# Optimization experiments

Hardware: AMD Instinct MI355X
Metric: run time of the kernel (lower is better)

The kernel has to match this reference:

```python
import jax, jax.numpy as jnp
import numpy as np
from jax.scipy.special import logsumexp

EPS = 0.05        # entropic regularization (blur^p)
N_ITERS = 20      # Sinkhorn iterations
N, M, D = 8192, 8192, 64


def setup_inputs() -> dict:
    key = jax.random.key(0)
    k1, k2, k3, k4 = jax.random.split(key, 4)
    return {
        "a": jax.random.uniform(k1, (N,), dtype=jnp.float32),
        "x": jax.random.normal(k2, (N, D), dtype=jnp.float32),
        "b": jax.random.uniform(k3, (M,), dtype=jnp.float32),
        "y": jax.random.normal(k4, (M, D), dtype=jnp.float32),
    }


def reference(a, x, b, y):
    eps = EPS
    # _normalize_weights: probability simplex
    a = a / jnp.sum(a)
    b = b / jnp.sum(b)
    loga = jnp.log(a)
    logb = jnp.log(b)
    # squared-Euclidean cost C_ij = ||x_i - y_j||^2, built via one GEMM (online kernel's math)
    x2 = jnp.sum(x * x, axis=1)            # [N]
    y2 = jnp.sum(y * y, axis=1)            # [M]
    C = x2[:, None] + y2[None, :] - 2.0 * (x @ y.T)   # [N, M]

    # log-domain Sinkhorn: f_i = -eps * LSE_j( log b_j + (g_j - C_ij)/eps )
    def softmin_rows(g_, C_, logw):   # reduce over columns j -> [N]
        return -eps * logsumexp(logw[None, :] + (g_[None, :] - C_) / eps, axis=1)

    def softmin_cols(f_, C_, logw):   # reduce over rows i -> [M]
        return -eps * logsumexp(logw[:, None] + (f_[:, None] - C_) / eps, axis=0)

    def body(i, fg):
        f_, g_ = fg
        f_ = softmin_rows(g_, C, logb)
        g_ = softmin_cols(f_, C, loga)
        return (f_, g_)

    f0 = jnp.zeros_like(a)
    g0 = jnp.zeros_like(b)
    f, g = jax.lax.fori_loop(0, N_ITERS, body, (f0, g0))

    # GeomLoss-style: one final symmetric update from detached potentials (Danskin)
    f_d = jax.lax.stop_gradient(f)
    g_d = jax.lax.stop_gradient(g)
    f_fin = softmin_rows(g_d, C, logb)
    g_fin = softmin_cols(f_d, C, loga)
    # OT_eps(a, b) = <a, f> + <b, g>
    return jnp.sum(a * f_fin) + jnp.sum(b * g_fin)
```

## Files before the change

### kernel.cpp

```cpp
#include <hip/hip_runtime.h>
#include <hip/hip_bf16.h>

#define EPS       0.05f
#define N_ITERS   20
#define NR        8192
#define DIM       64
#define LOG2E     1.4426950408889634f
#define LN2       0.6931471805599453f
#define S2        (2.0f * LOG2E / EPS)
#define EPSLN2    (EPS * LN2)
#define NEGINF    (-1e30f)
#define NSPLIT    16

typedef __attribute__((ext_vector_type(8))) short short8;
typedef __attribute__((ext_vector_type(4))) float float4v;

#define GLD_LDS16(src, dst)                                              \
    __builtin_amdgcn_global_load_lds(                                    \
        (const __attribute__((address_space(1))) void*)(src),            \
        (__attribute__((address_space(3))) void*)(dst), 16, 0, 0)

__device__ __forceinline__ float wave_reduce_sum(float v) {
    #pragma unroll
    for (int m = 1; m < 64; m <<= 1) v += __shfl_xor(v, m, 64);
    return v;
}

__device__ __forceinline__ float merge16_l(const float2* __restrict__ P, int i) {
    float2 p[NSPLIT];
    float M = NEGINF;
    #pragma unroll
    for (int k = 0; k < NSPLIT; k++) {
        p[k] = P[k * NR + i];
        M = fmaxf(M, p[k].x);
    }
    float S = 0.f;
    #pragma unroll
    for (int k = 0; k < NSPLIT; k++)
        S += p[k].y * __builtin_amdgcn_exp2f(p[k].x - M);
    return M + __builtin_amdgcn_logf(S);
}

__global__ void sums_kernel(const float* __restrict__ a, const float* __restrict__ b,
                            float* __restrict__ sums) {
    __shared__ float red[32];
    int tid = threadIdx.x;
    float pa = 0.f, pb = 0.f;
    for (int i = tid; i < NR; i += blockDim.x) { pa += a[i]; pb += b[i]; }
    pa = wave_reduce_sum(pa);
    pb = wave_reduce_sum(pb);
    int wid = tid >> 6, ln = tid & 63;
    if (ln == 0) { red[wid] = pa; red[wid + 16] = pb; }
    __syncthreads();
    if (tid == 0) {
        float sa = 0.f, sb = 0.f;
        int nw = blockDim.x >> 6;
        for (int w = 0; w < nw; w++) { sa += red[w]; sb += red[w + 16]; }
        sums[0] = logf(sa); sums[1] = logf(sb); sums[2] = sa; sums[3] = sb;
    }
}

__global__ void prep_kernel(const float* __restrict__ x, const float* __restrict__ y,
                            const float* __restrict__ a, const float* __restrict__ b,
                            const float* __restrict__ sums,
                            short8* __restrict__ xs, short8* __restrict__ ys,
                            float* __restrict__ x2, float* __restrict__ y2,
                            float* __restrict__ la2, float* __restrict__ lb2,
                            float2* __restrict__ Pb) {
    int gid = blockIdx.x * 256 + threadIdx.x;
    bool isx = gid < NR * 8;
    int cid = isx ? gid : gid - NR * 8;
    int row = cid >> 3;
    int c   = cid & 7;
    const float4* src = (const float4*)(isx ? x : y);
    float4 v0 = src[row * 16 + c * 2];
    float4 v1 = src[row * 16 + c * 2 + 1];

    const float sc = isx ? S2 : 1.0f;
    short8 st;
    st[0] = __bfloat16_as_short(__float2bfloat16(v0.x * sc));
    st[1] = __bfloat16_as_short(__float2bfloat16(v0.y * sc));
    st[2] = __bfloat16_as_short(__float2bfloat16(v0.z * sc));
    st[3] = __bfloat16_as_short(__float2bfloat16(v0.w * sc));
    st[4] = __bfloat16_as_short(__float2bfloat16(v1.x * sc));
    st[5] = __bfloat16_as_short(__float2bfloat16(v1.y * sc));
    st[6] = __bfloat16_as_short(__float2bfloat16(v1.z * sc));
    st[7] = __bfloat16_as_short(__float2bfloat16(v1.w * sc));

    int T = row >> 4, ln = row & 15, f = c >> 2, q = c & 3;
    (isx ? xs : ys)[T * 128 + f * 64 + q * 16 + ln] = st;

    float sq = v0.x*v0.x + v0.y*v0.y + v0.z*v0.z + v0.w*v0.w
             + v1.x*v1.x + v1.y*v1.y + v1.z*v1.z + v1.w*v1.w;
    #pragma unroll
    for (int m = 1; m < 8; m <<= 1) sq += __shfl_xor(sq, m, 64);

    if (c == 0) {
        if (isx) {
            x2[row] = sq;
            la2[row] = (logf(a[row]) - sums[0]) * LOG2E;
        } else {
            y2[row] = sq;
            lb2[row] = (logf(b[row]) - sums[1]) * LOG2E;
            Pb[row] = make_float2(sq * (LOG2E / EPS), 1.0f);
            #pragma unroll
            for (int k = 1; k < NSPLIT; k++)
                Pb[k * NR + row] = make_float2(NEGINF, 0.0f);
        }
    }
}

#define LSE4(acc, mm, ss)                                                \
    {                                                                    \
        float z0 = (acc)[0], z1 = (acc)[1];                              \
        float z2 = (acc)[2], z3 = (acc)[3];                              \
        float mn = fmaxf(fmaxf(fmaxf(z0, z1), fmaxf(z2, z3)), (mm));     \
        float e  = __builtin_amdgcn_exp2f((mm) - mn);                    \
        float p  = (__builtin_amdgcn_exp2f(z0 - mn)                      \
                  + __builtin_amdgcn_exp2f(z1 - mn))                     \
                 + (__builtin_amdgcn_exp2f(z2 - mn)                      \
                  + __builtin_amdgcn_exp2f(z3 - mn));                    \
        (ss) = fmaf((ss), e, p);                                         \
        (mm) = mn;                                                       \
    }

__global__ __launch_bounds__(1024, 4) void pass_kernel(
        const short8* __restrict__ matXs,
        const short8* __restrict__ matYs,
        const float2* __restrict__ Pin,
        const float* __restrict__ lw2col,
        float2* __restrict__ Pout) {
    __shared__ __attribute__((aligned(16))) char xlds[65536];
    __shared__ __attribute__((aligned(16))) char ybuf[4][16384];
    __shared__ __attribute__((aligned(16))) float cbl[512];
    __shared__ float2 comb[512][5];

    const int tid = threadIdx.x;
    const int bi  = blockIdx.x;
    const int q   = bi & 15;
    const int rg  = bi >> 4;
    const int rb  = rg * 512;
    const int cb0 = q * 512;

    const int w    = tid >> 6;
    const int lane = tid & 63;
    const int quad = lane >> 4;
    const int ln   = lane & 15;
    const int cst  = w & 3;
    const int rq   = w >> 2;

    const char* xsrc = (const char*)matXs + (size_t)rb * 128;
    #pragma unroll
    for (int r = 0; r < 4; r++)
        GLD_LDS16(xsrc + r * 16384 + tid * 16, &xlds[r * 16384 + w * 1024]);
    const char* ysrc = (const char*)matYs + (size_t)cb0 * 128;
    #pragma unroll
    for (int c = 0; c < 4; c++)
        GLD_LDS16(ysrc + c * 16384 + tid * 16, &ybuf[c][w * 1024]);
    __builtin_amdgcn_sched_barrier(0);

    if (tid < 512) {
        int j = cb0 + tid;
        cbl[tid] = lw2col[j] - merge16_l(Pin, j);
    }
    __builtin_amdgcn_sched_barrier(0);
    __builtin_amdgcn_s_waitcnt(0x0073);
    __builtin_amdgcn_s_barrier();
    __builtin_amdgcn_sched_barrier(0);

    short8 xf0[8], xf1[8];
    {
        const char* xw = &xlds[(rq * 8) * 2048];
        #pragma unroll
        for (int t = 0; t < 8; t++) {
            xf0[t] = *(const short8*)(xw + t * 2048 + lane * 16);
            xf1[t] = *(const short8*)(xw + t * 2048 + 1024 + lane * 16);
        }
    }

    float lm[8], ls[8];
    #pragma unroll
    for (int t = 0; t < 8; t++) { lm[t] = NEGINF; ls[t] = 0.f; }

    #pragma unroll
    for (int c = 0; c < 4; c++) {
        const char* base = &ybuf[c][0];
        #pragma unroll
        for (int uu = 0; uu < 2; uu++) {
            const int u = cst * 2 + uu;
            short8 ya0 = *(const short8*)(base + u * 2048 + lane * 16);
            short8 ya1 = *(const short8*)(base + u * 2048 + 1024 + lane * 16);
            float4v cin = *(const float4v*)(cbl + (c * 8 + u) * 16 + quad * 4);

            #pragma unroll
            for (int tt = 0; tt < 8; tt++) {
                float4v acc = __builtin_amdgcn_mfma_f32_16x16x32_bf16(ya0, xf0[tt], cin, 0, 0, 0);
                acc = __builtin_amdgcn_mfma_f32_16x16x32_bf16(ya1, xf1[tt], acc, 0, 0, 0);
                LSE4(acc, lm[tt], ls[tt]);
            }
        }
        if (c < 3) {
            __builtin_amdgcn_sched_barrier(0);
            if (c == 0)      __builtin_amdgcn_s_waitcnt(0x0072);
            else if (c == 1) __builtin_amdgcn_s_waitcnt(0x0071);
            else             __builtin_amdgcn_s_waitcnt(0x0070);
            __builtin_amdgcn_s_barrier();
            __builtin_amdgcn_sched_barrier(0);
        }
    }

    #pragma unroll
    for (int mask = 16; mask < 64; mask <<= 1) {
        #pragma unroll
        for (int t = 0; t < 8; t++) {
            float mo = __shfl_xor(lm[t], mask, 64);
            float so = __shfl_xor(ls[t], mask, 64);
            float M  = fmaxf(lm[t], mo);
            ls[t] = ls[t] * __builtin_amdgcn_exp2f(lm[t] - M)
                  + so    * __builtin_amdgcn_exp2f(mo    - M);
            lm[t] = M;
        }
    }

    __syncthreads();
    if (lane < 16) {
        #pragma unroll
        for (int t = 0; t < 8; t++)
            comb[rq * 128 + t * 16 + ln][cst] = make_float2(lm[t], ls[t]);
    }
    __syncthreads();

    if (tid < 512) {
        float2 cc0 = comb[tid][0];
        float M = cc0.x, S = cc0.y;
        #pragma unroll
        for (int cc = 1; cc < 4; cc++) {
            float2 p = comb[tid][cc];
            float Mn = fmaxf(M, p.x);
            S = S * __builtin_amdgcn_exp2f(M - Mn)
              + p.y * __builtin_amdgcn_exp2f(p.x - Mn);
            M = Mn;
        }
        Pout[q * NR + rb + tid] = make_float2(M, S);
    }
}

__global__ void reduce1_kernel(const float* __restrict__ a, const float* __restrict__ b,
                               const float* __restrict__ x2, const float* __restrict__ y2,
                               const float2* __restrict__ Pff, const float2* __restrict__ Pgf,
                               float2* __restrict__ red2) {
    __shared__ float red[4];
    int tid = threadIdx.x;
    int r   = blockIdx.x * 128 + (tid & 127);
    bool gs = tid >= 128;
    float L  = merge16_l(gs ? Pgf : Pff, r);
    float sq = gs ? y2[r] : x2[r];
    float wv = gs ? b[r]  : a[r];
    float v  = wv * (sq - EPSLN2 * L);
    v = wave_reduce_sum(v);
    if ((tid & 63) == 0) red[tid >> 6] = v;
    __syncthreads();
    if (tid == 0) red2[blockIdx.x] = make_float2(red[0] + red[1], red[2] + red[3]);
}

__global__ void reduce2_kernel(const float* __restrict__ sums,
                               const float2* __restrict__ red2,
                               float* __restrict__ out) {
    int tid = threadIdx.x;
    float2 v = red2[tid];
    float da = wave_reduce_sum(v.x);
    float db = wave_reduce_sum(v.y);
    if (tid == 0) out[0] = da / sums[2] + db / sums[3];
}

extern "C" void kernel_launch(void* const* d_in, const int* in_sizes, int n_in,
                              void* d_out, int out_size, void* d_ws, size_t ws_size,
                              hipStream_t stream) {
    const float* a = (const float*)d_in[0];
    const float* x = (const float*)d_in[1];
    const float* b = (const float*)d_in[2];
    const float* y = (const float*)d_in[3];

    char* ws = (char*)d_ws;
    short8* xs = (short8*)ws;
    short8* ys = (short8*)(ws + (1 << 20));
    float* fp  = (float*)(ws + (2 << 20));
    float* x2  = fp;
    float* y2  = fp + NR;
    float* la2 = fp + 2 * NR;
    float* lb2 = fp + 3 * NR;
    float2* P   = (float2*)(fp + 4 * NR);
    float2* Pf  = P;
    float2* Pb  = P + NSPLIT * NR;
    float2* Pff = P + 2 * NSPLIT * NR;
    float2* Pgf = P + 3 * NSPLIT * NR;
    float2* red2 = P + 4 * NSPLIT * NR;
    float* sums  = (float*)(red2 + 64);

    sums_kernel<<<1, 1024, 0, stream>>>(a, b, sums);
    prep_kernel<<<(2 * NR * 8) / 256, 256, 0, stream>>>(x, y, a, b, sums,
                                                        xs, ys,
                                                        x2, y2, la2, lb2, Pb);

    for (int it = 0; it < N_ITERS; it++) {
        pass_kernel<<<256, 1024, 0, stream>>>(xs, ys, Pb, lb2, Pf);
        pass_kernel<<<256, 1024, 0, stream>>>(ys, xs, Pf, la2, Pb);
    }
    pass_kernel<<<256, 1024, 0, stream>>>(xs, ys, Pb, lb2, Pff);
    pass_kernel<<<256, 1024, 0, stream>>>(ys, xs, Pf, la2, Pgf);

    reduce1_kernel<<<64, 256, 0, stream>>>(a, b, x2, y2, Pff, Pgf, red2);
    reduce2_kernel<<<1, 64, 0, stream>>>(sums, red2, (float*)d_out);
}
```

Measured before the change: 864.7 us.

## Fuse all Sinkhorn passes into one persistent cooperative kernel with grid barriers

Replaces the 42 separate pass launches and two reduction kernels with a single cooperative kernel. Each block keeps its 512-row x tile and 512-row y tile resident in LDS for every pass and swaps their roles between f and g updates, with a software grid barrier between passes. This removes launch overhead and the repeated global-to-LDS reloads of x and y. In exchange it adds atomic-based grid synchronisation, needs all 256 blocks co-resident, and halves the waves working on each column slice.

```diff
diff --git a/kernel.cpp b/kernel.cpp
--- a/kernel.cpp
+++ b/kernel.cpp
@@ -11,6 +11,7 @@
 #define EPSLN2    (EPS * LN2)
 #define NEGINF    (-1e30f)
 #define NSPLIT    16
+#define NPASS     (2 * N_ITERS + 2)
 
 typedef __attribute__((ext_vector_type(8))) short short8;
 typedef __attribute__((ext_vector_type(4))) float float4v;
@@ -26,7 +27,7 @@
     return v;
 }
 
-__device__ __forceinline__ float merge16_l(const float2* __restrict__ P, int i) {
+__device__ __forceinline__ float merge16_l(const float2* P, int i) {
     float2 p[NSPLIT];
     float M = NEGINF;
     #pragma unroll
@@ -41,8 +42,31 @@
     return M + __builtin_amdgcn_logf(S);
 }
 
+__device__ __forceinline__ void gsync(unsigned* sv) {
+    __syncthreads();
+    if (threadIdx.x == 0) {
+        __threadfence();
+        unsigned g = __hip_atomic_load(&sv[1], __ATOMIC_RELAXED,
+                                       __HIP_MEMORY_SCOPE_AGENT);
+        unsigned a = __hip_atomic_fetch_add(&sv[0], 1u, __ATOMIC_ACQ_REL,
+                                            __HIP_MEMORY_SCOPE_AGENT);
+        if (a == 255u) {
+            __hip_atomic_store(&sv[0], 0u, __ATOMIC_RELAXED,
+                               __HIP_MEMORY_SCOPE_AGENT);
+            __hip_atomic_store(&sv[1], g + 1u, __ATOMIC_RELEASE,
+                               __HIP_MEMORY_SCOPE_AGENT);
+        } else {
+            while (__hip_atomic_load(&sv[1], __ATOMIC_RELAXED,
+                                     __HIP_MEMORY_SCOPE_AGENT) == g)
+                __builtin_amdgcn_s_sleep(1);
+        }
+        __threadfence();
+    }
+    __syncthreads();
+}
+
 __global__ void sums_kernel(const float* __restrict__ a, const float* __restrict__ b,
-                            float* __restrict__ sums) {
+                            float* __restrict__ sums, unsigned* __restrict__ sv) {
     __shared__ float red[32];
     int tid = threadIdx.x;
     float pa = 0.f, pb = 0.f;
@@ -57,6 +81,7 @@
         int nw = blockDim.x >> 6;
         for (int w = 0; w < nw; w++) { sa += red[w]; sb += red[w + 16]; }
         sums[0] = logf(sa); sums[1] = logf(sb); sums[2] = sa; sums[3] = sb;
+        sv[0] = 0u; sv[1] = 0u;
     }
 }
 
@@ -124,153 +149,135 @@
         (mm) = mn;                                                       \
     }
 
-__global__ __launch_bounds__(1024, 4) void pass_kernel(
-        const short8* __restrict__ matXs,
-        const short8* __restrict__ matYs,
-        const float2* __restrict__ Pin,
-        const float* __restrict__ lw2col,
-        float2* __restrict__ Pout) {
-    __shared__ __attribute__((aligned(16))) char xlds[65536];
-    __shared__ __attribute__((aligned(16))) char ybuf[4][16384];
+__global__ __launch_bounds__(1024, 4) void sink_kernel(
+        const short8* __restrict__ xs, const short8* __restrict__ ys,
+        const float* __restrict__ la2, const float* __restrict__ lb2,
+        float2* P,
+        const float* __restrict__ a, const float* __restrict__ b,
+        const float* __restrict__ x2, const float* __restrict__ y2,
+        float2* red2, const float* __restrict__ sums,
+        unsigned* sv, float* out) {
+    __shared__ __attribute__((aligned(16))) char mlds[131072];
     __shared__ __attribute__((aligned(16))) float cbl[512];
-    __shared__ float2 comb[512][5];
+    __shared__ float2 comb[512][3];
 
     const int tid = threadIdx.x;
     const int bi  = blockIdx.x;
-    const int q   = bi & 15;
-    const int rg  = bi >> 4;
-    const int rb  = rg * 512;
-    const int cb0 = q * 512;
-
-    const int w    = tid >> 6;
-    const int lane = tid & 63;
-    const int quad = lane >> 4;
-    const int ln   = lane & 15;
-    const int cst  = w & 3;
-    const int rq   = w >> 2;
-
-    const char* xsrc = (const char*)matXs + (size_t)rb * 128;
-    #pragma unroll
-    for (int r = 0; r < 4; r++)
-        GLD_LDS16(xsrc + r * 16384 + tid * 16, &xlds[r * 16384 + w * 1024]);
-    const char* ysrc = (const char*)matYs + (size_t)cb0 * 128;
-    #pragma unroll
-    for (int c = 0; c < 4; c++)
-        GLD_LDS16(ysrc + c * 16384 + tid * 16, &ybuf[c][w * 1024]);
-    __builtin_amdgcn_sched_barrier(0);
-
-    if (tid < 512) {
-        int j = cb0 + tid;
-        cbl[tid] = lw2col[j] - merge16_l(Pin, j);
-    }
-    __builtin_amdgcn_sched_barrier(0);
-    __builtin_amdgcn_s_waitcnt(0x0073);
-    __builtin_amdgcn_s_barrier();
-    __builtin_amdgcn_sched_barrier(0);
-
-    short8 xf0[8], xf1[8];
-    {
-        const char* xw = &xlds[(rq * 8) * 2048];
+    const int ib  = bi >> 4, jb = bi & 15;
+    const int w   = tid >> 6, lane = tid & 63;
+    const int quad = lane >> 4, ln = lane & 15;
+    const int cst = w & 1, rq = w >> 1;
+
+    float2* Pf  = P;
+    float2* Pb  = P + NSPLIT * NR;
+    float2* Pff = P + 2 * NSPLIT * NR;
+    float2* Pgf = P + 3 * NSPLIT * NR;
+
+    const char* xsrc = (const char*)xs + (size_t)(ib * 512) * 128;
+    const char* ysrc = (const char*)ys + (size_t)(jb * 512) * 128;
+    #pragma unroll
+    for (int r = 0; r < 4; r++) {
+        GLD_LDS16(xsrc + r * 16384 + tid * 16, &mlds[r * 16384 + w * 1024]);
+        GLD_LDS16(ysrc + r * 16384 + tid * 16, &mlds[65536 + r * 16384 + w * 1024]);
+    }
+
+    for (int p = 0; p < NPASS; p++) {
+        const bool fs = (p < 2 * N_ITERS) ? !(p & 1) : (p == 2 * N_ITERS);
+        const float2* Pin = fs ? Pb : Pf;
+        float2* Pout = fs ? (p == 2 * N_ITERS     ? Pff : Pf)
+                          : (p == 2 * N_ITERS + 1 ? Pgf : Pb);
+        const float* lw  = fs ? lb2 : la2;
+        const int colbase = 512 * (fs ? jb : ib);
+        const int outidx  = fs ? (jb * NR + 512 * ib) : (ib * NR + 512 * jb);
+        const int roff = fs ? 0 : 65536;
+        const int coff = fs ? 65536 : 0;
+
+        if (tid < 512) {
+            int jj = colbase + tid;
+            cbl[tid] = lw[jj] - merge16_l(Pin, jj);
+        }
+        __syncthreads();
+
+        short8 rf0[4], rf1[4];
+        {
+            const char* rw = &mlds[roff + rq * 8192];
+            #pragma unroll
+            for (int t = 0; t < 4; t++) {
+                rf0[t] = *(const short8*)(rw + t * 2048 + lane * 16);
+                rf1[t] = *(const short8*)(rw + t * 2048 + 1024 + lane * 16);
+            }
+        }
+
+        float lm[4], ls[4];
         #pragma unroll
-        for (int t = 0; t < 8; t++) {
-            xf0[t] = *(const short8*)(xw + t * 2048 + lane * 16);
-            xf1[t] = *(const short8*)(xw + t * 2048 + 1024 + lane * 16);
-        }
-    }
-
-    float lm[8], ls[8];
-    #pragma unroll
-    for (int t = 0; t < 8; t++) { lm[t] = NEGINF; ls[t] = 0.f; }
-
-    #pragma unroll
-    for (int c = 0; c < 4; c++) {
-        const char* base = &ybuf[c][0];
-        #pragma unroll
-        for (int uu = 0; uu < 2; uu++) {
-            const int u = cst * 2 + uu;
-            short8 ya0 = *(const short8*)(base + u * 2048 + lane * 16);
-            short8 ya1 = *(const short8*)(base + u * 2048 + 1024 + lane * 16);
-            float4v cin = *(const float4v*)(cbl + (c * 8 + u) * 16 + quad * 4);
-
-            #pragma unroll
-            for (int tt = 0; tt < 8; tt++) {
-                float4v acc = __builtin_amdgcn_mfma_f32_16x16x32_bf16(ya0, xf0[tt], cin, 0, 0, 0);
-                acc = __builtin_amdgcn_mfma_f32_16x16x32_bf16(ya1, xf1[tt], acc, 0, 0, 0);
+        for (int t = 0; t < 4; t++) { lm[t] = NEGINF; ls[t] = 0.f; }
+
+        const char* cw = &mlds[coff + cst * 32768];
+        const float* cbw = cbl + cst * 256;
+        #pragma unroll 4
+        for (int u = 0; u < 16; u++) {
+            short8 ya0 = *(const short8*)(cw + u * 2048 + lane * 16);
+            short8 ya1 = *(const short8*)(cw + u * 2048 + 1024 + lane * 16);
+            float4v cin = *(const float4v*)(cbw + u * 16 + quad * 4);
+            #pragma unroll
+            for (int tt = 0; tt < 4; tt++) {
+                float4v acc = __builtin_amdgcn_mfma_f32_16x16x32_bf16(ya0, rf0[tt], cin, 0, 0, 0);
+                acc = __builtin_amdgcn_mfma_f32_16x16x32_bf16(ya1, rf1[tt], acc, 0, 0, 0);
                 LSE4(acc, lm[tt], ls[tt]);
             }
         }
-        if (c < 3) {
-            __builtin_amdgcn_sched_barrier(0);
-            if (c == 0)      __builtin_amdgcn_s_waitcnt(0x0072);
-            else if (c == 1) __builtin_amdgcn_s_waitcnt(0x0071);
-            else             __builtin_amdgcn_s_waitcnt(0x0070);
-            __builtin_amdgcn_s_barrier();
-            __builtin_amdgcn_sched_barrier(0);
-        }
-    }
-
-    #pragma unroll
-    for (int mask = 16; mask < 64; mask <<= 1) {
+
         #pragma unroll
-        for (int t = 0; t < 8; t++) {
-            float mo = __shfl_xor(lm[t], mask, 64);
-            float so = __shfl_xor(ls[t], mask, 64);
-            float M  = fmaxf(lm[t], mo);
-            ls[t] = ls[t] * __builtin_amdgcn_exp2f(lm[t] - M)
-                  + so    * __builtin_amdgcn_exp2f(mo    - M);
-            lm[t] = M;
-        }
-    }
-
+        for (int mask = 16; mask < 64; mask <<= 1) {
+            #pragma unroll
+            for (int t = 0; t < 4; t++) {
+                float mo = __shfl_xor(lm[t], mask, 64);
+                float so = __shfl_xor(ls[t], mask, 64);
+                float M  = fmaxf(lm[t], mo);
+                ls[t] = ls[t] * __builtin_amdgcn_exp2f(lm[t] - M)
+                      + so    * __builtin_amdgcn_exp2f(mo    - M);
+                lm[t] = M;
+            }
+        }
+
+        if (lane < 16) {
+            #pragma unroll
+            for (int t = 0; t < 4; t++)
+                comb[rq * 64 + t * 16 + ln][cst] = make_float2(lm[t], ls[t]);
+        }
+        __syncthreads();
+
+        if (tid < 512) {
+            float2 c0 = comb[tid][0], c1 = comb[tid][1];
+            float M = fmaxf(c0.x, c1.x);
+            float S = c0.y * __builtin_amdgcn_exp2f(c0.x - M)
+                    + c1.y * __builtin_amdgcn_exp2f(c1.x - M);
+            Pout[outidx + tid] = make_float2(M, S);
+        }
+        gsync(sv);
+    }
+
+    if (bi < 64 && tid < 256) {
+        int r = bi * 128 + (tid & 127);
+        bool gsd = tid >= 128;
+        float L  = merge16_l(gsd ? Pgf : Pff, r);
+        float sq = gsd ? y2[r] : x2[r];
+        float wv = gsd ? b[r]  : a[r];
+        float v  = wv * (sq - EPSLN2 * L);
+        v = wave_reduce_sum(v);
+        if ((tid & 63) == 0) cbl[tid >> 6] = v;
+    }
     __syncthreads();
-    if (lane < 16) {
-        #pragma unroll
-        for (int t = 0; t < 8; t++)
-            comb[rq * 128 + t * 16 + ln][cst] = make_float2(lm[t], ls[t]);
-    }
-    __syncthreads();
-
-    if (tid < 512) {
-        float2 cc0 = comb[tid][0];
-        float M = cc0.x, S = cc0.y;
-        #pragma unroll
-        for (int cc = 1; cc < 4; cc++) {
-            float2 p = comb[tid][cc];
-            float Mn = fmaxf(M, p.x);
-            S = S * __builtin_amdgcn_exp2f(M - Mn)
-              + p.y * __builtin_amdgcn_exp2f(p.x - Mn);
-            M = Mn;
-        }
-        Pout[q * NR + rb + tid] = make_float2(M, S);
-    }
-}
-
-__global__ void reduce1_kernel(const float* __restrict__ a, const float* __restrict__ b,
-                               const float* __restrict__ x2, const float* __restrict__ y2,
-                               const float2* __restrict__ Pff, const float2* __restrict__ Pgf,
-                               float2* __restrict__ red2) {
-    __shared__ float red[4];
-    int tid = threadIdx.x;
-    int r   = blockIdx.x * 128 + (tid & 127);
-    bool gs = tid >= 128;
-    float L  = merge16_l(gs ? Pgf : Pff, r);
-    float sq = gs ? y2[r] : x2[r];
-    float wv = gs ? b[r]  : a[r];
-    float v  = wv * (sq - EPSLN2 * L);
-    v = wave_reduce_sum(v);
-    if ((tid & 63) == 0) red[tid >> 6] = v;
-    __syncthreads();
-    if (tid == 0) red2[blockIdx.x] = make_float2(red[0] + red[1], red[2] + red[3]);
-}
-
-__global__ void reduce2_kernel(const float* __restrict__ sums,
-                               const float2* __restrict__ red2,
-                               float* __restrict__ out) {
-    int tid = threadIdx.x;
-    float2 v = red2[tid];
-    float da = wave_reduce_sum(v.x);
-    float db = wave_reduce_sum(v.y);
-    if (tid == 0) out[0] = da / sums[2] + db / sums[3];
+    if (bi < 64 && tid == 0)
+        red2[bi] = make_float2(cbl[0] + cbl[1], cbl[2] + cbl[3]);
+    gsync(sv);
+
+    if (bi == 0 && tid < 64) {
+        float2 v = red2[tid];
+        float da = wave_reduce_sum(v.x);
+        float db = wave_reduce_sum(v.y);
+        if (tid == 0) out[0] = da / sums[2] + db / sums[3];
+    }
 }
 
 extern "C" void kernel_launch(void* const* d_in, const int* in_sizes, int n_in,
@@ -290,25 +297,20 @@
     float* la2 = fp + 2 * NR;
     float* lb2 = fp + 3 * NR;
     float2* P   = (float2*)(fp + 4 * NR);
-    float2* Pf  = P;
-    float2* Pb  = P + NSPLIT * NR;
-    float2* Pff = P + 2 * NSPLIT * NR;
-    float2* Pgf = P + 3 * NSPLIT * NR;
     float2* red2 = P + 4 * NSPLIT * NR;
     float* sums  = (float*)(red2 + 64);
-
-    sums_kernel<<<1, 1024, 0, stream>>>(a, b, sums);
+    unsigned* sv = (unsigned*)(sums + 4);
+    float* outp  = (float*)d_out;
+
+    sums_kernel<<<1, 1024, 0, stream>>>(a, b, sums, sv);
     prep_kernel<<<(2 * NR * 8) / 256, 256, 0, stream>>>(x, y, a, b, sums,
                                                         xs, ys,
-                                                        x2, y2, la2, lb2, Pb);
-
-    for (int it = 0; it < N_ITERS; it++) {
-        pass_kernel<<<256, 1024, 0, stream>>>(xs, ys, Pb, lb2, Pf);
-        pass_kernel<<<256, 1024, 0, stream>>>(ys, xs, Pf, la2, Pb);
-    }
-    pass_kernel<<<256, 1024, 0, stream>>>(xs, ys, Pb, lb2, Pff);
-    pass_kernel<<<256, 1024, 0, stream>>>(ys, xs, Pf, la2, Pgf);
-
-    reduce1_kernel<<<64, 256, 0, stream>>>(a, b, x2, y2, Pff, Pgf, red2);
-    reduce2_kernel<<<1, 64, 0, stream>>>(sums, red2, (float*)d_out);
-}
+                                                        x2, y2, la2, lb2,
+                                                        P + NSPLIT * NR);
+
+    void* args[] = { (void*)&xs, (void*)&ys, (void*)&la2, (void*)&lb2,
+                     (void*)&P, (void*)&a, (void*)&b, (void*)&x2, (void*)&y2,
+                     (void*)&red2, (void*)&sums, (void*)&sv, (void*)&outp };
+    hipLaunchCooperativeKernel((void*)sink_kernel, dim3(256), dim3(1024),
+                               args, 0, stream);
+}
```

Result: slower. 1.865 ms (+115.7%).

## Halve pass block to 512 threads, 256 rows, load x fragments directly

Applied to the files above, without the earlier changes.

Each pass kernel block now covers 256 rows by 512 columns with 512 threads, launched as 512 blocks instead of 256. Wave x fragments are read straight from global memory into registers rather than staged through LDS. The y tile is loaded in one shot and consumed after a single barrier, which drops the staged waitcnt pipelining over four y chunks. The aim is to double the block count for better CU coverage and cut LDS and register footprint per block. The cost is loss of load/compute overlap and more redundant y-tile loads across blocks.

```diff
diff --git a/kernel.cpp b/kernel.cpp
--- a/kernel.cpp
+++ b/kernel.cpp
@@ -124,95 +124,73 @@
         (mm) = mn;                                                       \
     }
 
-__global__ __launch_bounds__(1024, 4) void pass_kernel(
+__global__ __launch_bounds__(512, 4) void pass_kernel(
         const short8* __restrict__ matXs,
         const short8* __restrict__ matYs,
         const float2* __restrict__ Pin,
         const float* __restrict__ lw2col,
         float2* __restrict__ Pout) {
-    __shared__ __attribute__((aligned(16))) char xlds[65536];
-    __shared__ __attribute__((aligned(16))) char ybuf[4][16384];
+    __shared__ __attribute__((aligned(16))) char ylds[65536];
     __shared__ __attribute__((aligned(16))) float cbl[512];
-    __shared__ float2 comb[512][5];
+    __shared__ float2 comb[256][3];
 
     const int tid = threadIdx.x;
     const int bi  = blockIdx.x;
     const int q   = bi & 15;
     const int rg  = bi >> 4;
-    const int rb  = rg * 512;
+    const int rb  = rg * 256;
     const int cb0 = q * 512;
 
     const int w    = tid >> 6;
     const int lane = tid & 63;
     const int quad = lane >> 4;
     const int ln   = lane & 15;
-    const int cst  = w & 3;
-    const int rq   = w >> 2;
-
-    const char* xsrc = (const char*)matXs + (size_t)rb * 128;
-    #pragma unroll
-    for (int r = 0; r < 4; r++)
-        GLD_LDS16(xsrc + r * 16384 + tid * 16, &xlds[r * 16384 + w * 1024]);
+    const int cst  = w & 1;
+    const int rq   = w >> 1;
+
     const char* ysrc = (const char*)matYs + (size_t)cb0 * 128;
     #pragma unroll
-    for (int c = 0; c < 4; c++)
-        GLD_LDS16(ysrc + c * 16384 + tid * 16, &ybuf[c][w * 1024]);
-    __builtin_amdgcn_sched_barrier(0);
-
-    if (tid < 512) {
+    for (int k = 0; k < 8; k++)
+        GLD_LDS16(ysrc + k * 8192 + tid * 16, &ylds[k * 8192 + w * 1024]);
+
+    const char* xsrc = (const char*)matXs + (size_t)rb * 128
+                     + (size_t)(rq * 4) * 2048 + (size_t)lane * 16;
+    short8 xf0[4], xf1[4];
+    #pragma unroll
+    for (int t = 0; t < 4; t++) {
+        xf0[t] = *(const short8*)(xsrc + t * 2048);
+        xf1[t] = *(const short8*)(xsrc + t * 2048 + 1024);
+    }
+
+    {
         int j = cb0 + tid;
         cbl[tid] = lw2col[j] - merge16_l(Pin, j);
     }
-    __builtin_amdgcn_sched_barrier(0);
-    __builtin_amdgcn_s_waitcnt(0x0073);
-    __builtin_amdgcn_s_barrier();
-    __builtin_amdgcn_sched_barrier(0);
-
-    short8 xf0[8], xf1[8];
-    {
-        const char* xw = &xlds[(rq * 8) * 2048];
+    __syncthreads();
+
+    float lm[4], ls[4];
+    #pragma unroll
+    for (int t = 0; t < 4; t++) { lm[t] = NEGINF; ls[t] = 0.f; }
+
+    const char* cw  = &ylds[cst * 32768];
+    const float* cbw = cbl + cst * 256;
+    #pragma unroll 4
+    for (int u = 0; u < 16; u++) {
+        short8 ya0 = *(const short8*)(cw + u * 2048 + lane * 16);
+        short8 ya1 = *(const short8*)(cw + u * 2048 + 1024 + lane * 16);
+        float4v cin = *(const float4v*)(cbw + u * 16 + quad * 4);
         #pragma unroll
-        for (int t = 0; t < 8; t++) {
-            xf0[t] = *(const short8*)(xw + t * 2048 + lane * 16);
-            xf1[t] = *(const short8*)(xw + t * 2048 + 1024 + lane * 16);
-        }
-    }
-
-    float lm[8], ls[8];
-    #pragma unroll
-    for (int t = 0; t < 8; t++) { lm[t] = NEGINF; ls[t] = 0.f; }
-
-    #pragma unroll
-    for (int c = 0; c < 4; c++) {
-        const char* base = &ybuf[c][0];
-        #pragma unroll
-        for (int uu = 0; uu < 2; uu++) {
-            const int u = cst * 2 + uu;
-            short8 ya0 = *(const short8*)(base + u * 2048 + lane * 16);
-            short8 ya1 = *(const short8*)(base + u * 2048 + 1024 + lane * 16);
-            float4v cin = *(const float4v*)(cbl + (c * 8 + u) * 16 + quad * 4);
-
-            #pragma unroll
-            for (int tt = 0; tt < 8; tt++) {
-                float4v acc = __builtin_amdgcn_mfma_f32_16x16x32_bf16(ya0, xf0[tt], cin, 0, 0, 0);
-                acc = __builtin_amdgcn_mfma_f32_16x16x32_bf16(ya1, xf1[tt], acc, 0, 0, 0);
-                LSE4(acc, lm[tt], ls[tt]);
-            }
-        }
-        if (c < 3) {
-            __builtin_amdgcn_sched_barrier(0);
-            if (c == 0)      __builtin_amdgcn_s_waitcnt(0x0072);
-            else if (c == 1) __builtin_amdgcn_s_waitcnt(0x0071);
-            else             __builtin_amdgcn_s_waitcnt(0x0070);
-            __builtin_amdgcn_s_barrier();
-            __builtin_amdgcn_sched_barrier(0);
+        for (int tt = 0; tt < 4; tt++) {
+            float4v acc = __builtin_amdgcn_mfma_f32_16x16x32_bf16(ya0, xf0[tt], cin, 0, 0, 0);
+            acc = __builtin_amdgcn_mfma_f32_16x16x32_bf16(ya1, xf1[tt], acc, 0, 0, 0);
+            LSE4(acc, lm[tt], ls[tt]);
         }
     }
 
     #pragma unroll
     for (int mask = 16; mask < 64; mask <<= 1) {
         #pragma unroll
-        for (int t = 0; t < 8; t++) {
+        for (int t = 0; t < 4; t++) {
             float mo = __shfl_xor(lm[t], mask, 64);
             float so = __shfl_xor(ls[t], mask, 64);
             float M  = fmaxf(lm[t], mo);
@@ -222,25 +200,18 @@
         }
     }
 
-    __syncthreads();
     if (lane < 16) {
         #pragma unroll
-        for (int t = 0; t < 8; t++)
-            comb[rq * 128 + t * 16 + ln][cst] = make_float2(lm[t], ls[t]);
-    }
-    __syncthreads();
-
-    if (tid < 512) {
-        float2 cc0 = comb[tid][0];
-        float M = cc0.x, S = cc0.y;
-        #pragma unroll
-        for (int cc = 1; cc < 4; cc++) {
-            float2 p = comb[tid][cc];
-            float Mn = fmaxf(M, p.x);
-            S = S * __builtin_amdgcn_exp2f(M - Mn)
-              + p.y * __builtin_amdgcn_exp2f(p.x - Mn);
-            M = Mn;
-        }
+        for (int t = 0; t < 4; t++)
+            comb[rq * 64 + t * 16 + ln][cst] = make_float2(lm[t], ls[t]);
+    }
+    __syncthreads();
+
+    if (tid < 256) {
+        float2 c0 = comb[tid][0], c1 = comb[tid][1];
+        float M = fmaxf(c0.x, c1.x);
+        float S = c0.y * __builtin_amdgcn_exp2f(c0.x - M)
+                + c1.y * __builtin_amdgcn_exp2f(c1.x - M);
         Pout[q * NR + rb + tid] = make_float2(M, S);
     }
 }
@@ -303,11 +274,11 @@
                                                         x2, y2, la2, lb2, Pb);
 
     for (int it = 0; it < N_ITERS; it++) {
-        pass_kernel<<<256, 1024, 0, stream>>>(xs, ys, Pb, lb2, Pf);
-        pass_kernel<<<256, 1024, 0, stream>>>(ys, xs, Pf, la2, Pb);
-    }
-    pass_kernel<<<256, 1024, 0, stream>>>(xs, ys, Pb, lb2, Pff);
-    pass_kernel<<<256, 1024, 0, stream>>>(ys, xs, Pf, la2, Pgf);
+        pass_kernel<<<512, 512, 0, stream>>>(xs, ys, Pb, lb2, Pf);
+        pass_kernel<<<512, 512, 0, stream>>>(ys, xs, Pf, la2, Pb);
+    }
+    pass_kernel<<<512, 512, 0, stream>>>(xs, ys, Pb, lb2, Pff);
+    pass_kernel<<<512, 512, 0, stream>>>(ys, xs, Pf, la2, Pgf);
 
     reduce1_kernel<<<64, 256, 0, stream>>>(a, b, x2, y2, Pff, Pgf, red2);
     reduce2_kernel<<<1, 64, 0, stream>>>(sums, red2, (float*)d_out);
```

Measured after the change: 885.4 us. 2.4% more time.
